# Kernel optimization log

Measured on AMD Instinct MI355X. Metric: run time of the kernel, lower is better.

The kernel has to match this reference:

```python
import jax, jax.numpy as jnp
import numpy as np

B, S, D, H = 2, 2048, 512, 8
HD = D // H
SPARSITY = 0.15
KTOP = max(1, int(S * SPARSITY))          # 307 important rows
HALF_WIN = min(32, S // 4) // 2           # 16 -> window |i-j| <= 16
RC = min(16, S // 8)                      # 16 random links per query token


def setup_inputs() -> dict:
    key = jax.random.key(0)
    ks = jax.random.split(key, 8)
    s = 0.02
    return {
        "x":  jax.random.normal(ks[0], (B, S, D), jnp.float32),
        "Wq": jax.random.normal(ks[1], (D, D), jnp.float32) * s,
        "bq": jnp.zeros((D,), jnp.float32),
        "Wk": jax.random.normal(ks[2], (D, D), jnp.float32) * s,
        "bk": jnp.zeros((D,), jnp.float32),
        "Wv": jax.random.normal(ks[3], (D, D), jnp.float32) * s,
        "bv": jnp.zeros((D,), jnp.float32),
        "Wo": jax.random.normal(ks[4], (D, D), jnp.float32) * s,
        "bo": jnp.zeros((D,), jnp.float32),
        "Ws1": jax.random.normal(ks[5], (D, D // 2), jnp.float32) * s,
        "bs1": jnp.zeros((D // 2,), jnp.float32),
        "Ws2": jax.random.normal(ks[6], (D // 2, 1), jnp.float32) * s,
        "bs2": jnp.zeros((1,), jnp.float32),
        # models torch.randperm(S)[:RC] per (b, i); duplicates are harmless for set-to-1
        "rand_idx": jax.random.randint(ks[7], (B, S, RC), 0, S, jnp.int32),
    }


def _sparse_mask(x, Ws1, bs1, Ws2, bs2, rand_idx):
    # importance scorer: Linear -> ReLU -> Linear -> Sigmoid, squeeze(-1)
    imp = jax.nn.sigmoid(jax.nn.relu(x @ Ws1 + bs1) @ Ws2 + bs2)[..., 0]  # [B,S]
    _, top_idx = jax.lax.top_k(imp, KTOP)                                  # [B,KTOP]
    brange = jnp.arange(B)
    row_imp = jnp.zeros((B, S), bool).at[brange[:, None], top_idx].set(True)
    idx = jnp.arange(S)
    win = jnp.abs(idx[:, None] - idx[None, :]) <= HALF_WIN                 # [S,S]
    rmask = jnp.zeros((B, S, S), bool).at[
        brange[:, None, None], idx[None, :, None], rand_idx].set(True)    # [B,S,S]
    mask = row_imp[:, :, None] | win[None, :, :] | rmask                   # [B,S,S]
    tril = idx[:, None] >= idx[None, :]                                    # causal (mask * (causal==0))
    return mask & tril


def reference(x, Wq, bq, Wk, bk, Wv, bv, Wo, bo, Ws1, bs1, Ws2, bs2, rand_idx):
    allowed = _sparse_mask(x, Ws1, bs1, Ws2, bs2, rand_idx)                # [B,S,S] bool
    q = (x @ Wq + bq).reshape(B, S, H, HD).transpose(0, 2, 1, 3)           # [B,H,S,HD]
    k = (x @ Wk + bk).reshape(B, S, H, HD).transpose(0, 2, 1, 3)
    v = (x @ Wv + bv).reshape(B, S, H, HD).transpose(0, 2, 1, 3)
    scores = jnp.einsum('bhid,bhjd->bhij', q, k) / jnp.sqrt(jnp.float32(HD))
    scores = jnp.where(allowed[:, None, :, :], scores, -jnp.inf)
    attn = jax.nn.softmax(scores, axis=-1)                                 # every row has j=i allowed
    out = jnp.einsum('bhij,bhjd->bhid', attn, v)
    out = out.transpose(0, 2, 1, 3).reshape(B, S, D)
    return out @ Wo + bo
```

## Files before the change

kernel.cpp:

```cpp
#include <hip/hip_runtime.h>
#include <math.h>

typedef unsigned short u16;
typedef unsigned int u32;
typedef unsigned long long u64;
typedef short bf16x8 __attribute__((ext_vector_type(8)));
typedef float f32x4 __attribute__((ext_vector_type(4)));

constexpr int NB = 2, NS = 2048, ND = 512, NH = 8, NHD = 64;
constexpr int NKTOP = 307, NHWIN = 16, NRC = 16;
constexpr int NILIST = 320;
constexpr int NCHUNK = 4;
constexpr int NKMAX = 33;
constexpr int LDSPAD = 40;

__device__ __forceinline__ u16 f2bf(float f) {
  u32 u = __builtin_bit_cast(u32, f);
  u32 r = (u + 0x7FFFu + ((u >> 16) & 1u)) >> 16;
  return (u16)r;
}
__device__ __forceinline__ float bf2f(short v) {
  return __builtin_bit_cast(float, (u32)(u16)v << 16);
}

__global__ __launch_bounds__(256) void csa_cvt_x(const float* __restrict__ x, u16* __restrict__ xb) {
  int i = (blockIdx.x * 256 + threadIdx.x) * 4;
  float4 v = *(const float4*)(x + i);
  u32 o0 = (u32)f2bf(v.x) | ((u32)f2bf(v.y) << 16);
  u32 o1 = (u32)f2bf(v.z) | ((u32)f2bf(v.w) << 16);
  *(uint2*)(xb + i) = make_uint2(o0, o1);
}

__global__ __launch_bounds__(256) void csa_cvt_w(const float* __restrict__ W0, const float* __restrict__ W1,
                                                 const float* __restrict__ W2, const float* __restrict__ W3,
                                                 u16* __restrict__ wt) {
  __shared__ float tile[32][33];
  int w = blockIdx.z;
  const float* src = (w == 0) ? W0 : (w == 1) ? W1 : (w == 2) ? W2 : W3;
  int kb = blockIdx.x * 32, nb = blockIdx.y * 32;
  int tx = threadIdx.x & 31, ty = threadIdx.x >> 5;
  for (int i = ty; i < 32; i += 8) tile[i][tx] = src[(size_t)(kb + i) * ND + nb + tx];
  __syncthreads();
  u16* dst = wt + (size_t)w * ND * ND;
  for (int i = ty; i < 32; i += 8) dst[(size_t)(nb + i) * ND + kb + tx] = f2bf(tile[tx][i]);
}

__global__ __launch_bounds__(256) void csa_scorer_gemm(const float* __restrict__ A, const float* __restrict__ Bw,
                                                       const float* __restrict__ bias, float* __restrict__ Hout) {
  __shared__ float As[16][64];
  __shared__ float Bs[16][64];
  const int tid = threadIdx.x;
  const int m0 = blockIdx.x * 64;
  const int n0 = blockIdx.y * 64;
  const int ty = tid >> 4, tx = tid & 15;
  float acc[4][4] = {};
  const int lrow = tid & 63, lkq = (tid >> 6) * 4;
  const int lkk = tid >> 4, lc4 = (tid & 15) * 4;
  for (int k0 = 0; k0 < ND; k0 += 16) {
    __syncthreads();
    float4 a = *(const float4*)(&A[(size_t)(m0 + lrow) * ND + k0 + lkq]);
    As[lkq + 0][lrow] = a.x; As[lkq + 1][lrow] = a.y; As[lkq + 2][lrow] = a.z; As[lkq + 3][lrow] = a.w;
    *(float4*)(&Bs[lkk][lc4]) = *(const float4*)(&Bw[(size_t)(k0 + lkk) * 256 + n0 + lc4]);
    __syncthreads();
    for (int k = 0; k < 16; k++) {
      float4 av = *(const float4*)(&As[k][ty * 4]);
      float4 bv = *(const float4*)(&Bs[k][tx * 4]);
      float aa[4] = {av.x, av.y, av.z, av.w};
      float bb[4] = {bv.x, bv.y, bv.z, bv.w};
      for (int i = 0; i < 4; i++)
        for (int j = 0; j < 4; j++)
          acc[i][j] += aa[i] * bb[j];
    }
  }
  for (int i = 0; i < 4; i++) {
    int m = m0 + ty * 4 + i;
    for (int j = 0; j < 4; j++) {
      int n = n0 + tx * 4 + j;
      Hout[(size_t)m * 256 + n] = fmaxf(acc[i][j] + bias[n], 0.f);
    }
  }
}

__global__ __launch_bounds__(256) void csa_logit(const float* __restrict__ Hout, const float* __restrict__ Ws2,
                                                 const float* __restrict__ bs2, float* __restrict__ imp) {
  const int wave = threadIdx.x >> 6, lane = threadIdx.x & 63;
  const int row = blockIdx.x * 4 + wave;
  float4 h = *(const float4*)(&Hout[(size_t)row * 256 + lane * 4]);
  float4 w = *(const float4*)(&Ws2[lane * 4]);
  float s = h.x * w.x + h.y * w.y + h.z * w.z + h.w * w.w;
  for (int off = 1; off < 64; off <<= 1) s += __shfl_xor(s, off, 64);
  if (lane == 0) imp[row] = 1.f / (1.f + __expf(-(s + bs2[0])));
}

__global__ __launch_bounds__(256) void csa_rank(const float* __restrict__ imp, int* __restrict__ rowimp) {
  __shared__ float vals[NS];
  const int b = blockIdx.y;
  {
    int t8 = threadIdx.x * 8;
    *(float4*)(&vals[t8]) = *(const float4*)(&imp[b * NS + t8]);
    *(float4*)(&vals[t8 + 4]) = *(const float4*)(&imp[b * NS + t8 + 4]);
  }
  __syncthreads();
  const int wave = threadIdx.x >> 6, lane = threadIdx.x & 63;
  const int s0 = blockIdx.x * 8 + wave * 2;
  const int s1 = s0 + 1;
  const float v0 = vals[s0], v1 = vals[s1];
  int r0 = 0, r1 = 0;
  for (int t = lane; t < NS; t += 64) {
    float u = vals[t];
    r0 += (int)((u > v0) | ((u == v0) & (t < s0)));
    r1 += (int)((u > v1) | ((u == v1) & (t < s1)));
  }
  for (int off = 1; off < 64; off <<= 1) {
    r0 += __shfl_xor(r0, off, 64);
    r1 += __shfl_xor(r1, off, 64);
  }
  if (lane == 0) {
    rowimp[b * NS + s0] = (r0 < NKTOP) ? 1 : 0;
    rowimp[b * NS + s1] = (r1 < NKTOP) ? 1 : 0;
  }
}

__global__ __launch_bounds__(256) void csa_ilist(const int* __restrict__ rowimp, int* __restrict__ ilist) {
  __shared__ int cs[256];
  int b = blockIdx.x, t = threadIdx.x;
  int flags[8], sum = 0;
  for (int k = 0; k < 8; k++) {
    flags[k] = rowimp[b * NS + t * 8 + k];
    sum += flags[k];
  }
  cs[t] = sum;
  __syncthreads();
  for (int off = 1; off < 256; off <<= 1) {
    int v = (t >= off) ? cs[t - off] : 0;
    __syncthreads();
    cs[t] += v;
    __syncthreads();
  }
  int pos = cs[t] - sum;
  for (int k = 0; k < 8; k++)
    if (flags[k]) ilist[b * NILIST + pos++] = t * 8 + k;
  if (t < NILIST - NKTOP) ilist[b * NILIST + NKTOP + t] = -1;
}

__global__ __launch_bounds__(256) void csa_gemm_qkv(const u16* __restrict__ A, const u16* __restrict__ Bt,
                                                    const float* __restrict__ bq, const float* __restrict__ bk,
                                                    const float* __restrict__ bv, u16* __restrict__ qb,
                                                    u16* __restrict__ kb, u16* __restrict__ vtb,
                                                    u16* __restrict__ vb) {
  __shared__ __attribute__((aligned(16))) u16 As[64 * LDSPAD];
  __shared__ __attribute__((aligned(16))) u16 Bs[64 * LDSPAD];
  const int tid = threadIdx.x;
  const int wave = tid >> 6, lane = tid & 63;
  const int quad = lane >> 4, col = lane & 15;
  const int m0 = blockIdx.x * 64;
  const int n0 = blockIdx.y * 64;
  const f32x4 zf = {0.f, 0.f, 0.f, 0.f};
  f32x4 acc[4] = {zf, zf, zf, zf};
  const int lrow = tid >> 2, lk = (tid & 3) * 8;
  for (int k0 = 0; k0 < ND; k0 += 32) {
    __syncthreads();
    *(uint4*)(&As[lrow * LDSPAD + lk]) = *(const uint4*)(&A[(size_t)(m0 + lrow) * ND + k0 + lk]);
    *(uint4*)(&Bs[lrow * LDSPAD + lk]) = *(const uint4*)(&Bt[(size_t)(n0 + lrow) * ND + k0 + lk]);
    __syncthreads();
    bf16x8 af = *(const bf16x8*)(&As[(wave * 16 + col) * LDSPAD + quad * 8]);
    for (int nt = 0; nt < 4; nt++) {
      bf16x8 bfr = *(const bf16x8*)(&Bs[(nt * 16 + col) * LDSPAD + quad * 8]);
      acc[nt] = __builtin_amdgcn_mfma_f32_16x16x32_bf16(af, bfr, acc[nt], 0, 0, 0);
    }
  }
  const int w = n0 >> 9;
  const float* bias = (w == 0) ? bq : (w == 1) ? bk : bv;
  for (int nt = 0; nt < 4; nt++) {
    const int ng = n0 + nt * 16 + col;
    const int nn = ng & 511, hh = nn >> 6, hd = nn & 63;
    const float bvv = bias[nn];
    for (int r = 0; r < 4; r++) {
      const int m = m0 + wave * 16 + quad * 4 + r;
      const int bb = m >> 11, s = m & (NS - 1);
      u16 v16 = f2bf(acc[nt][r] + bvv);
      if (w == 0) qb[((size_t)(bb * NH + hh) * NS + s) * NHD + hd] = v16;
      else if (w == 1) kb[((size_t)(bb * NH + hh) * NS + s) * NHD + hd] = v16;
      else {
        vtb[((size_t)(bb * NH + hh) * NHD + hd) * NS + s] = v16;
        vb[((size_t)(bb * NH + hh) * NS + s) * NHD + hd] = v16;
      }
    }
  }
}

__global__ __launch_bounds__(256) void csa_gemm_out(const u16* __restrict__ A, const u16* __restrict__ Bt,
                                                    const float* __restrict__ bias, float* __restrict__ outp) {
  __shared__ __attribute__((aligned(16))) u16 As[64 * LDSPAD];
  __shared__ __attribute__((aligned(16))) u16 Bs[64 * LDSPAD];
  const int tid = threadIdx.x;
  const int wave = tid >> 6, lane = tid & 63;
  const int quad = lane >> 4, col = lane & 15;
  const int m0 = blockIdx.x * 64;
  const int n0 = blockIdx.y * 64;
  const f32x4 zf = {0.f, 0.f, 0.f, 0.f};
  f32x4 acc[4] = {zf, zf, zf, zf};
  const int lrow = tid >> 2, lk = (tid & 3) * 8;
  for (int k0 = 0; k0 < ND; k0 += 32) {
    __syncthreads();
    *(uint4*)(&As[lrow * LDSPAD + lk]) = *(const uint4*)(&A[(size_t)(m0 + lrow) * ND + k0 + lk]);
    *(uint4*)(&Bs[lrow * LDSPAD + lk]) = *(const uint4*)(&Bt[(size_t)(n0 + lrow) * ND + k0 + lk]);
    __syncthreads();
    bf16x8 af = *(const bf16x8*)(&As[(wave * 16 + col) * LDSPAD + quad * 8]);
    for (int nt = 0; nt < 4; nt++) {
      bf16x8 bfr = *(const bf16x8*)(&Bs[(nt * 16 + col) * LDSPAD + quad * 8]);
      acc[nt] = __builtin_amdgcn_mfma_f32_16x16x32_bf16(af, bfr, acc[nt], 0, 0, 0);
    }
  }
  for (int nt = 0; nt < 4; nt++) {
    const int n = n0 + nt * 16 + col;
    const float bvv = bias[n];
    for (int r = 0; r < 4; r++) {
      const int m = m0 + wave * 16 + quad * 4 + r;
      outp[(size_t)m * ND + n] = acc[nt][r] + bvv;
    }
  }
}

__global__ __launch_bounds__(64) void csa_attn_imp(const u16* __restrict__ qb, const u16* __restrict__ kb,
                                                   const u16* __restrict__ vtb, const int* __restrict__ ilist,
                                                   float* __restrict__ pbuf) {
  const int lane = threadIdx.x;
  const int quad = lane >> 4, col = lane & 15;
  const int qt = blockIdx.x;
  const int chunk = blockIdx.y;
  const int bh = blockIdx.z;
  const int b = bh >> 3, h = bh & 7;

  const int* il = ilist + b * NILIST;
  const u16* qptr = qb + (size_t)(b * NH + h) * NS * NHD;
  const u16* kptr = kb + (size_t)(b * NH + h) * NS * NHD;
  const u16* vptr = vtb + (size_t)(b * NH + h) * NHD * NS;

  const int iq = il[qt * 16 + col];
  const int qrow = (iq < 0) ? 0 : iq;
  bf16x8 qf0 = *(const bf16x8*)(qptr + qrow * NHD + quad * 8);
  bf16x8 qf1 = *(const bf16x8*)(qptr + qrow * NHD + 32 + quad * 8);

  const f32x4 zf = {0.f, 0.f, 0.f, 0.f};
  float m_r[4], l_r[4];
  f32x4 of[4];
  int irow[4];
  for (int r = 0; r < 4; r++) {
    m_r[r] = -INFINITY;
    l_r[r] = 0.f;
    irow[r] = il[qt * 16 + quad * 4 + r];
  }
  for (int n = 0; n < 4; n++) of[n] = zf;

  __shared__ __attribute__((aligned(16))) u16 Pl[16 * LDSPAD];

  const int max_i = il[(qt * 16 + 15 > NKTOP - 1) ? (NKTOP - 1) : (qt * 16 + 15)];
  const int ntiles = (max_i >> 5) + 1;
  for (int t = chunk; t < ntiles; t += NCHUNK) {
    const int j0 = t * 32;
    f32x4 c0 = zf, c1 = zf;
    {
      bf16x8 k00 = *(const bf16x8*)(kptr + (j0 + col) * NHD + quad * 8);
      bf16x8 k01 = *(const bf16x8*)(kptr + (j0 + col) * NHD + 32 + quad * 8);
      c0 = __builtin_amdgcn_mfma_f32_16x16x32_bf16(qf0, k00, c0, 0, 0, 0);
      c0 = __builtin_amdgcn_mfma_f32_16x16x32_bf16(qf1, k01, c0, 0, 0, 0);
      bf16x8 k10 = *(const bf16x8*)(kptr + (j0 + 16 + col) * NHD + quad * 8);
      bf16x8 k11 = *(const bf16x8*)(kptr + (j0 + 16 + col) * NHD + 32 + quad * 8);
      c1 = __builtin_amdgcn_mfma_f32_16x16x32_bf16(qf0, k10, c1, 0, 0, 0);
      c1 = __builtin_amdgcn_mfma_f32_16x16x32_bf16(qf1, k11, c1, 0, 0, 0);
    }
    const int j_0 = j0 + col, j_1 = j0 + 16 + col;
    float p0s[4], p1s[4], alpha[4];
    for (int r = 0; r < 4; r++) {
      const int i = irow[r];
      float s0 = (j_0 <= i) ? c0[r] * 0.125f : -INFINITY;
      float s1 = (j_1 <= i) ? c1[r] * 0.125f : -INFINITY;
      float vmax = fmaxf(s0, s1);
      for (int off = 1; off < 16; off <<= 1) vmax = fmaxf(vmax, __shfl_xor(vmax, off, 64));
      float newm = fmaxf(m_r[r], vmax);
      bool dead = (newm == -INFINITY);
      float a = dead ? 1.f : __expf(m_r[r] - newm);
      float p0 = dead ? 0.f : __expf(s0 - newm);
      float p1 = dead ? 0.f : __expf(s1 - newm);
      float psum = p0 + p1;
      for (int off = 1; off < 16; off <<= 1) psum += __shfl_xor(psum, off, 64);
      m_r[r] = newm;
      l_r[r] = l_r[r] * a + psum;
      alpha[r] = a;
      p0s[r] = p0;
      p1s[r] = p1;
    }
    for (int n = 0; n < 4; n++)
      for (int r = 0; r < 4; r++) of[n][r] *= alpha[r];
    __syncthreads();
    for (int r = 0; r < 4; r++) {
      Pl[(quad * 4 + r) * LDSPAD + col] = f2bf(p0s[r]);
      Pl[(quad * 4 + r) * LDSPAD + 16 + col] = f2bf(p1s[r]);
    }
    __syncthreads();
    bf16x8 pf = *(const bf16x8*)(&Pl[col * LDSPAD + quad * 8]);
    for (int vn = 0; vn < 4; vn++) {
      bf16x8 vf = *(const bf16x8*)(vptr + (size_t)(vn * 16 + col) * NS + j0 + quad * 8);
      of[vn] = __builtin_amdgcn_mfma_f32_16x16x32_bf16(pf, vf, of[vn], 0, 0, 0);
    }
  }
  float* pr = pbuf + ((size_t)(bh * NCHUNK + chunk) * NILIST + qt * 16) * 66;
  for (int r = 0; r < 4; r++) {
    const int row = quad * 4 + r;
    if (col == 0) {
      pr[row * 66 + 0] = m_r[r];
      pr[row * 66 + 1] = l_r[r];
    }
    for (int vn = 0; vn < 4; vn++)
      pr[row * 66 + 2 + vn * 16 + col] = of[vn][r];
  }
}

__global__ __launch_bounds__(64) void csa_merge(const float* __restrict__ pbuf, const int* __restrict__ ilist,
                                                u16* __restrict__ attnb) {
  const int kp = blockIdx.x, h = blockIdx.y, b = blockIdx.z;
  const int lane = threadIdx.x;
  const int z = b * NH + h;
  float mc[NCHUNK], lc[NCHUNK], mstar = -INFINITY;
  for (int c = 0; c < NCHUNK; c++) {
    const float* base = pbuf + ((size_t)(z * NCHUNK + c) * NILIST + kp) * 66;
    mc[c] = base[0];
    lc[c] = base[1];
    mstar = fmaxf(mstar, mc[c]);
  }
  float lsum = 0.f, osum = 0.f;
  for (int c = 0; c < NCHUNK; c++) {
    const float* base = pbuf + ((size_t)(z * NCHUNK + c) * NILIST + kp) * 66;
    float w = (mc[c] == -INFINITY) ? 0.f : __expf(mc[c] - mstar);
    lsum += w * lc[c];
    osum += w * base[2 + lane];
  }
  const int i = ilist[b * NILIST + kp];
  attnb[((size_t)(b * NS + i) * NH + h) * NHD + lane] = f2bf(osum / lsum);
}

__global__ __launch_bounds__(256) void csa_attn_sparse(const u16* __restrict__ qb, const u16* __restrict__ kb,
                                                       const u16* __restrict__ vb, const int* __restrict__ rowimp,
                                                       const int* __restrict__ rand_idx, u16* __restrict__ attnb) {
  __shared__ __attribute__((aligned(16))) u16 ql[4][64];
  __shared__ float pl[4][64];
  __shared__ int jl[4][64];
  const int wave = threadIdx.x >> 6, lane = threadIdx.x & 63;
  const int i = blockIdx.x * 4 + wave;
  const int h = blockIdx.y, b = blockIdx.z;
  const int imp = rowimp[b * NS + i];

  const u16* qrow = qb + ((size_t)(b * NH + h) * NS + i) * NHD;
  const u16* kbase = kb + (size_t)(b * NH + h) * NS * NHD;
  const u16* vbase = vb + (size_t)(b * NH + h) * NS * NHD;

  if (lane < 8) *(bf16x8*)(&ql[wave][lane * 8]) = *(const bf16x8*)(qrow + lane * 8);
  __syncthreads();

  int j = 0, valid = 0;
  if (lane < 17) {
    j = i - NHWIN + lane;
    valid = (j >= 0);
  } else if (lane < 17 + NRC) {
    const int* rr = rand_idx + ((size_t)b * NS + i) * NRC;
    int c = lane - 17;
    j = rr[c];
    valid = (j <= i - NHWIN - 1);
    for (int cp = 0; cp < c; cp++) valid &= (rr[cp] != j);
  }
  const int jr = valid ? j : 0;

  float s = 0.f;
  const u16* krow = kbase + (size_t)jr * NHD;
  for (int c8 = 0; c8 < 8; c8++) {
    bf16x8 kv = *(const bf16x8*)(krow + c8 * 8);
    bf16x8 qv = *(const bf16x8*)(&ql[wave][c8 * 8]);
    for (int e = 0; e < 8; e++) s += bf2f(qv[e]) * bf2f(kv[e]);
  }
  s = valid ? s * 0.125f : -INFINITY;

  float vmax = s;
  for (int off = 1; off < 64; off <<= 1) vmax = fmaxf(vmax, __shfl_xor(vmax, off, 64));
  float p = valid ? __expf(s - vmax) : 0.f;
  float lsum = p;
  for (int off = 1; off < 64; off <<= 1) lsum += __shfl_xor(lsum, off, 64);

  pl[wave][lane] = p;
  jl[wave][lane] = jr;
  __syncthreads();

  float o = 0.f;
  for (int jj = 0; jj < NKMAX; jj++) {
    float pj = pl[wave][jj];
    int jk = jl[wave][jj];
    o += pj * bf2f((short)vbase[(size_t)jk * NHD + lane]);
  }
  if (!imp)
    attnb[((size_t)(b * NS + i) * NH + h) * NHD + lane] = f2bf(o / lsum);
}

extern "C" void kernel_launch(void* const* d_in, const int* in_sizes, int n_in,
                              void* d_out, int out_size, void* d_ws, size_t ws_size,
                              hipStream_t stream) {
  const float* x = (const float*)d_in[0];
  const float* bq = (const float*)d_in[2];
  const float* bk = (const float*)d_in[4];
  const float* bv = (const float*)d_in[6];
  const float* bo = (const float*)d_in[8];
  const float* Ws1 = (const float*)d_in[9];
  const float* Ws2 = (const float*)d_in[11];
  const float* bs2 = (const float*)d_in[12];
  const int* rand_idx = (const int*)d_in[13];
  float* out = (float*)d_out;

  char* p = (char*)d_ws;
  u16* xb = (u16*)p;         p += (size_t)NB * NS * ND * 2;
  u16* wt = (u16*)p;         p += (size_t)4 * ND * ND * 2;
  u16* qbuf = (u16*)p;       p += (size_t)NB * NH * NS * NHD * 2;
  u16* kbuf = (u16*)p;       p += (size_t)NB * NH * NS * NHD * 2;
  u16* vtbuf = (u16*)p;      p += (size_t)NB * NH * NHD * NS * 2;
  u16* vbuf = (u16*)p;       p += (size_t)NB * NH * NS * NHD * 2;
  u16* attnb = (u16*)p;      p += (size_t)NB * NS * ND * 2;
  float* impbuf = (float*)p; p += (size_t)NB * NS * 4;
  int* rowimp = (int*)p;     p += (size_t)NB * NS * 4;
  int* ilist = (int*)p;      p += (size_t)NB * NILIST * 4;
  float* scratch = (float*)p;
  float* hbuf = scratch;
  float* pbuf = scratch;

  csa_cvt_x<<<dim3(NB * NS * ND / 1024), 256, 0, stream>>>(x, xb);
  csa_cvt_w<<<dim3(16, 16, 4), 256, 0, stream>>>((const float*)d_in[1], (const float*)d_in[3],
                                                 (const float*)d_in[5], (const float*)d_in[7], wt);

  csa_scorer_gemm<<<dim3(64, 4), 256, 0, stream>>>(x, Ws1, (const float*)d_in[10], hbuf);
  csa_logit<<<dim3(NB * NS / 4), 256, 0, stream>>>(hbuf, Ws2, bs2, impbuf);
  csa_rank<<<dim3(NS / 8, NB), 256, 0, stream>>>(impbuf, rowimp);
  csa_ilist<<<dim3(NB), 256, 0, stream>>>(rowimp, ilist);

  csa_gemm_qkv<<<dim3(64, 24), 256, 0, stream>>>(xb, wt, bq, bk, bv, qbuf, kbuf, vtbuf, vbuf);

  csa_attn_imp<<<dim3(NILIST / 16, NCHUNK, NB * NH), 64, 0, stream>>>(qbuf, kbuf, vtbuf, ilist, pbuf);
  csa_attn_sparse<<<dim3(NS / 4, NH, NB), 256, 0, stream>>>(qbuf, kbuf, vbuf, rowimp, rand_idx, attnb);
  csa_merge<<<dim3(NKTOP, NH, NB), 64, 0, stream>>>(pbuf, ilist, attnb);

  csa_gemm_out<<<dim3(64, 8), 256, 0, stream>>>(attnb, wt + 3 * (size_t)ND * ND, bo, out);
}
```

Baseline: 232.3 us.

## Fuse scorer MLP layers and fold x bf16 conversion into QKV GEMM

Merges the scorer's first GEMM, ReLU and second-layer dot product into one kernel that reduces partial logits with atomics, so the hidden activation buffer and the separate logit kernel are no longer needed. Ranking now runs on the raw logit instead of the sigmoid, which keeps the top-k order because sigmoid is monotonic. The x-to-bf16 conversion kernel is removed and the QKV GEMM reads fp32 x and converts while staging it in LDS, with the M tile raised to 128 rows. The cost is an extra memset, float atomics whose summation order can vary between runs, and twice the LDS traffic per block for the A tile.

```diff
diff --git a/kernel.cpp b/kernel.cpp
--- a/kernel.cpp
+++ b/kernel.cpp
@@ -21,14 +21,6 @@
 }
 __device__ __forceinline__ float bf2f(short v) {
   return __builtin_bit_cast(float, (u32)(u16)v << 16);
-}
-
-__global__ __launch_bounds__(256) void csa_cvt_x(const float* __restrict__ x, u16* __restrict__ xb) {
-  int i = (blockIdx.x * 256 + threadIdx.x) * 4;
-  float4 v = *(const float4*)(x + i);
-  u32 o0 = (u32)f2bf(v.x) | ((u32)f2bf(v.y) << 16);
-  u32 o1 = (u32)f2bf(v.z) | ((u32)f2bf(v.w) << 16);
-  *(uint2*)(xb + i) = make_uint2(o0, o1);
 }
 
 __global__ __launch_bounds__(256) void csa_cvt_w(const float* __restrict__ W0, const float* __restrict__ W1,
@@ -45,51 +37,49 @@
   for (int i = ty; i < 32; i += 8) dst[(size_t)(nb + i) * ND + kb + tx] = f2bf(tile[tx][i]);
 }
 
-__global__ __launch_bounds__(256) void csa_scorer_gemm(const float* __restrict__ A, const float* __restrict__ Bw,
-                                                       const float* __restrict__ bias, float* __restrict__ Hout) {
-  __shared__ float As[16][64];
-  __shared__ float Bs[16][64];
+__global__ __launch_bounds__(256) void csa_scorer(const float* __restrict__ x, const float* __restrict__ Ws1,
+                                                  const float* __restrict__ bs1, const float* __restrict__ Ws2,
+                                                  float* __restrict__ logit) {
+  __shared__ float As[32][33];
+  __shared__ float Bs[32][68];
   const int tid = threadIdx.x;
-  const int m0 = blockIdx.x * 64;
-  const int n0 = blockIdx.y * 64;
-  const int ty = tid >> 4, tx = tid & 15;
-  float acc[4][4] = {};
-  const int lrow = tid & 63, lkq = (tid >> 6) * 4;
-  const int lkk = tid >> 4, lc4 = (tid & 15) * 4;
-  for (int k0 = 0; k0 < ND; k0 += 16) {
-    __syncthreads();
-    float4 a = *(const float4*)(&A[(size_t)(m0 + lrow) * ND + k0 + lkq]);
-    As[lkq + 0][lrow] = a.x; As[lkq + 1][lrow] = a.y; As[lkq + 2][lrow] = a.z; As[lkq + 3][lrow] = a.w;
-    *(float4*)(&Bs[lkk][lc4]) = *(const float4*)(&Bw[(size_t)(k0 + lkk) * 256 + n0 + lc4]);
-    __syncthreads();
-    for (int k = 0; k < 16; k++) {
-      float4 av = *(const float4*)(&As[k][ty * 4]);
-      float4 bv = *(const float4*)(&Bs[k][tx * 4]);
-      float aa[4] = {av.x, av.y, av.z, av.w};
-      float bb[4] = {bv.x, bv.y, bv.z, bv.w};
-      for (int i = 0; i < 4; i++)
-        for (int j = 0; j < 4; j++)
-          acc[i][j] += aa[i] * bb[j];
-    }
-  }
-  for (int i = 0; i < 4; i++) {
-    int m = m0 + ty * 4 + i;
-    for (int j = 0; j < 4; j++) {
-      int n = n0 + tx * 4 + j;
-      Hout[(size_t)m * 256 + n] = fmaxf(acc[i][j] + bias[n], 0.f);
-    }
-  }
-}
-
-__global__ __launch_bounds__(256) void csa_logit(const float* __restrict__ Hout, const float* __restrict__ Ws2,
-                                                 const float* __restrict__ bs2, float* __restrict__ imp) {
-  const int wave = threadIdx.x >> 6, lane = threadIdx.x & 63;
-  const int row = blockIdx.x * 4 + wave;
-  float4 h = *(const float4*)(&Hout[(size_t)row * 256 + lane * 4]);
-  float4 w = *(const float4*)(&Ws2[lane * 4]);
-  float s = h.x * w.x + h.y * w.y + h.z * w.z + h.w * w.w;
-  for (int off = 1; off < 64; off <<= 1) s += __shfl_xor(s, off, 64);
-  if (lane == 0) imp[row] = 1.f / (1.f + __expf(-(s + bs2[0])));
+  const int m0 = blockIdx.x * 32, n0 = blockIdx.y * 64;
+  const int r2 = (tid >> 4) * 2;
+  const int c4 = (tid & 15) * 4;
+  float acc[2][4] = {};
+  const int arow = tid & 31, aks = (tid >> 5) * 4;
+  const int bk = tid >> 3, bc = (tid & 7) * 8;
+  for (int k0 = 0; k0 < ND; k0 += 32) {
+    __syncthreads();
+    float4 av = *(const float4*)(&x[(size_t)(m0 + arow) * ND + k0 + aks]);
+    As[aks + 0][arow] = av.x;
+    As[aks + 1][arow] = av.y;
+    As[aks + 2][arow] = av.z;
+    As[aks + 3][arow] = av.w;
+    *(float4*)(&Bs[bk][bc]) = *(const float4*)(&Ws1[(size_t)(k0 + bk) * 256 + n0 + bc]);
+    *(float4*)(&Bs[bk][bc + 4]) = *(const float4*)(&Ws1[(size_t)(k0 + bk) * 256 + n0 + bc + 4]);
+    __syncthreads();
+    for (int k = 0; k < 32; k++) {
+      float a0 = As[k][r2], a1 = As[k][r2 + 1];
+      float4 b = *(const float4*)(&Bs[k][c4]);
+      acc[0][0] += a0 * b.x; acc[0][1] += a0 * b.y; acc[0][2] += a0 * b.z; acc[0][3] += a0 * b.w;
+      acc[1][0] += a1 * b.x; acc[1][1] += a1 * b.y; acc[1][2] += a1 * b.z; acc[1][3] += a1 * b.w;
+    }
+  }
+  float4 w2 = *(const float4*)(&Ws2[n0 + c4]);
+  float4 b1 = *(const float4*)(&bs1[n0 + c4]);
+  float p0 = fmaxf(acc[0][0] + b1.x, 0.f) * w2.x + fmaxf(acc[0][1] + b1.y, 0.f) * w2.y +
+             fmaxf(acc[0][2] + b1.z, 0.f) * w2.z + fmaxf(acc[0][3] + b1.w, 0.f) * w2.w;
+  float p1 = fmaxf(acc[1][0] + b1.x, 0.f) * w2.x + fmaxf(acc[1][1] + b1.y, 0.f) * w2.y +
+             fmaxf(acc[1][2] + b1.z, 0.f) * w2.z + fmaxf(acc[1][3] + b1.w, 0.f) * w2.w;
+  for (int off = 1; off < 16; off <<= 1) {
+    p0 += __shfl_xor(p0, off, 64);
+    p1 += __shfl_xor(p1, off, 64);
+  }
+  if ((tid & 15) == 0) {
+    atomicAdd(&logit[m0 + r2], p0);
+    atomicAdd(&logit[m0 + r2 + 1], p1);
+  }
 }
 
 __global__ __launch_bounds__(256) void csa_rank(const float* __restrict__ imp, int* __restrict__ rowimp) {
@@ -143,47 +133,67 @@
   if (t < NILIST - NKTOP) ilist[b * NILIST + NKTOP + t] = -1;
 }
 
-__global__ __launch_bounds__(256) void csa_gemm_qkv(const u16* __restrict__ A, const u16* __restrict__ Bt,
+__global__ __launch_bounds__(256) void csa_gemm_qkv(const float* __restrict__ x, const u16* __restrict__ Bt,
                                                     const float* __restrict__ bq, const float* __restrict__ bk,
                                                     const float* __restrict__ bv, u16* __restrict__ qb,
                                                     u16* __restrict__ kb, u16* __restrict__ vtb,
                                                     u16* __restrict__ vb) {
-  __shared__ __attribute__((aligned(16))) u16 As[64 * LDSPAD];
+  __shared__ __attribute__((aligned(16))) u16 As[128 * LDSPAD];
   __shared__ __attribute__((aligned(16))) u16 Bs[64 * LDSPAD];
   const int tid = threadIdx.x;
   const int wave = tid >> 6, lane = tid & 63;
   const int quad = lane >> 4, col = lane & 15;
-  const int m0 = blockIdx.x * 64;
+  const int m0 = blockIdx.x * 128;
   const int n0 = blockIdx.y * 64;
   const f32x4 zf = {0.f, 0.f, 0.f, 0.f};
-  f32x4 acc[4] = {zf, zf, zf, zf};
-  const int lrow = tid >> 2, lk = (tid & 3) * 8;
+  f32x4 acc[2][4] = {{zf, zf, zf, zf}, {zf, zf, zf, zf}};
+  const int sar = tid >> 1, sak = (tid & 1) * 16;
+  const int sbr = tid >> 2, sbk = (tid & 3) * 8;
   for (int k0 = 0; k0 < ND; k0 += 32) {
     __syncthreads();
-    *(uint4*)(&As[lrow * LDSPAD + lk]) = *(const uint4*)(&A[(size_t)(m0 + lrow) * ND + k0 + lk]);
-    *(uint4*)(&Bs[lrow * LDSPAD + lk]) = *(const uint4*)(&Bt[(size_t)(n0 + lrow) * ND + k0 + lk]);
-    __syncthreads();
-    bf16x8 af = *(const bf16x8*)(&As[(wave * 16 + col) * LDSPAD + quad * 8]);
-    for (int nt = 0; nt < 4; nt++) {
-      bf16x8 bfr = *(const bf16x8*)(&Bs[(nt * 16 + col) * LDSPAD + quad * 8]);
-      acc[nt] = __builtin_amdgcn_mfma_f32_16x16x32_bf16(af, bfr, acc[nt], 0, 0, 0);
+    {
+      const float* xp = &x[(size_t)(m0 + sar) * ND + k0 + sak];
+      float4 v0 = *(const float4*)(xp), v1 = *(const float4*)(xp + 4);
+      float4 v2 = *(const float4*)(xp + 8), v3 = *(const float4*)(xp + 12);
+      u32 w0 = (u32)f2bf(v0.x) | ((u32)f2bf(v0.y) << 16);
+      u32 w1 = (u32)f2bf(v0.z) | ((u32)f2bf(v0.w) << 16);
+      u32 w2 = (u32)f2bf(v1.x) | ((u32)f2bf(v1.y) << 16);
+      u32 w3 = (u32)f2bf(v1.z) | ((u32)f2bf(v1.w) << 16);
+      u32 w4 = (u32)f2bf(v2.x) | ((u32)f2bf(v2.y) << 16);
+      u32 w5 = (u32)f2bf(v2.z) | ((u32)f2bf(v2.w) << 16);
+      u32 w6 = (u32)f2bf(v3.x) | ((u32)f2bf(v3.y) << 16);
+      u32 w7 = (u32)f2bf(v3.z) | ((u32)f2bf(v3.w) << 16);
+      u32* ap = (u32*)&As[sar * LDSPAD + sak];
+      ap[0] = w0; ap[1] = w1; ap[2] = w2; ap[3] = w3;
+      ap[4] = w4; ap[5] = w5; ap[6] = w6; ap[7] = w7;
+    }
+    *(uint4*)(&Bs[sbr * LDSPAD + sbk]) = *(const uint4*)(&Bt[(size_t)(n0 + sbr) * ND + k0 + sbk]);
+    __syncthreads();
+    bf16x8 af0 = *(const bf16x8*)(&As[(wave * 32 + col) * LDSPAD + quad * 8]);
+    bf16x8 af1 = *(const bf16x8*)(&As[(wave * 32 + 16 + col) * LDSPAD + quad * 8]);
+    for (int c = 0; c < 4; c++) {
+      bf16x8 bfr = *(const bf16x8*)(&Bs[(c * 16 + col) * LDSPAD + quad * 8]);
+      acc[0][c] = __builtin_amdgcn_mfma_f32_16x16x32_bf16(af0, bfr, acc[0][c], 0, 0, 0);
+      acc[1][c] = __builtin_amdgcn_mfma_f32_16x16x32_bf16(af1, bfr, acc[1][c], 0, 0, 0);
     }
   }
   const int w = n0 >> 9;
   const float* bias = (w == 0) ? bq : (w == 1) ? bk : bv;
-  for (int nt = 0; nt < 4; nt++) {
-    const int ng = n0 + nt * 16 + col;
+  for (int c = 0; c < 4; c++) {
+    const int ng = n0 + c * 16 + col;
     const int nn = ng & 511, hh = nn >> 6, hd = nn & 63;
     const float bvv = bias[nn];
-    for (int r = 0; r < 4; r++) {
-      const int m = m0 + wave * 16 + quad * 4 + r;
-      const int bb = m >> 11, s = m & (NS - 1);
-      u16 v16 = f2bf(acc[nt][r] + bvv);
-      if (w == 0) qb[((size_t)(bb * NH + hh) * NS + s) * NHD + hd] = v16;
-      else if (w == 1) kb[((size_t)(bb * NH + hh) * NS + s) * NHD + hd] = v16;
-      else {
-        vtb[((size_t)(bb * NH + hh) * NHD + hd) * NS + s] = v16;
-        vb[((size_t)(bb * NH + hh) * NS + s) * NHD + hd] = v16;
+    for (int r = 0; r < 2; r++) {
+      for (int rr = 0; rr < 4; rr++) {
+        const int m = m0 + wave * 32 + r * 16 + quad * 4 + rr;
+        const int bb = m >> 11, s = m & (NS - 1);
+        u16 v16 = f2bf(acc[r][c][rr] + bvv);
+        if (w == 0) qb[((size_t)(bb * NH + hh) * NS + s) * NHD + hd] = v16;
+        else if (w == 1) kb[((size_t)(bb * NH + hh) * NS + s) * NHD + hd] = v16;
+        else {
+          vtb[((size_t)(bb * NH + hh) * NHD + hd) * NS + s] = v16;
+          vb[((size_t)(bb * NH + hh) * NS + s) * NHD + hd] = v16;
+        }
       }
     }
   }
@@ -409,36 +419,32 @@
   const float* bv = (const float*)d_in[6];
   const float* bo = (const float*)d_in[8];
   const float* Ws1 = (const float*)d_in[9];
+  const float* bs1 = (const float*)d_in[10];
   const float* Ws2 = (const float*)d_in[11];
-  const float* bs2 = (const float*)d_in[12];
   const int* rand_idx = (const int*)d_in[13];
   float* out = (float*)d_out;
 
   char* p = (char*)d_ws;
-  u16* xb = (u16*)p;         p += (size_t)NB * NS * ND * 2;
   u16* wt = (u16*)p;         p += (size_t)4 * ND * ND * 2;
   u16* qbuf = (u16*)p;       p += (size_t)NB * NH * NS * NHD * 2;
   u16* kbuf = (u16*)p;       p += (size_t)NB * NH * NS * NHD * 2;
   u16* vtbuf = (u16*)p;      p += (size_t)NB * NH * NHD * NS * 2;
   u16* vbuf = (u16*)p;       p += (size_t)NB * NH * NS * NHD * 2;
   u16* attnb = (u16*)p;      p += (size_t)NB * NS * ND * 2;
-  float* impbuf = (float*)p; p += (size_t)NB * NS * 4;
+  float* logit = (float*)p;  p += (size_t)NB * NS * 4;
   int* rowimp = (int*)p;     p += (size_t)NB * NS * 4;
   int* ilist = (int*)p;      p += (size_t)NB * NILIST * 4;
-  float* scratch = (float*)p;
-  float* hbuf = scratch;
-  float* pbuf = scratch;
-
-  csa_cvt_x<<<dim3(NB * NS * ND / 1024), 256, 0, stream>>>(x, xb);
+  float* pbuf = (float*)p;
+
   csa_cvt_w<<<dim3(16, 16, 4), 256, 0, stream>>>((const float*)d_in[1], (const float*)d_in[3],
                                                  (const float*)d_in[5], (const float*)d_in[7], wt);
 
-  csa_scorer_gemm<<<dim3(64, 4), 256, 0, stream>>>(x, Ws1, (const float*)d_in[10], hbuf);
-  csa_logit<<<dim3(NB * NS / 4), 256, 0, stream>>>(hbuf, Ws2, bs2, impbuf);
-  csa_rank<<<dim3(NS / 8, NB), 256, 0, stream>>>(impbuf, rowimp);
+  (void)hipMemsetAsync(logit, 0, (size_t)NB * NS * 4, stream);
+  csa_scorer<<<dim3(NB * NS / 32, 4), 256, 0, stream>>>(x, Ws1, bs1, Ws2, logit);
+  csa_rank<<<dim3(NS / 8, NB), 256, 0, stream>>>(logit, rowimp);
   csa_ilist<<<dim3(NB), 256, 0, stream>>>(rowimp, ilist);
 
-  csa_gemm_qkv<<<dim3(64, 24), 256, 0, stream>>>(xb, wt, bq, bk, bv, qbuf, kbuf, vtbuf, vbuf);
+  csa_gemm_qkv<<<dim3(32, 24), 256, 0, stream>>>(x, wt, bq, bk, bv, qbuf, kbuf, vtbuf, vbuf);
 
   csa_attn_imp<<<dim3(NILIST / 16, NCHUNK, NB * NH), 64, 0, stream>>>(qbuf, kbuf, vtbuf, ilist, pbuf);
   csa_attn_sparse<<<dim3(NS / 4, NH, NB), 256, 0, stream>>>(qbuf, kbuf, vbuf, rowimp, rand_idx, attnb);
```

Measured after the change: 220.4 us. 1.05x faster.
